# Performance work log

Measured on AMD Instinct MI355X. Metric: run time of the kernel, lower is better.

## Reference

```python
import jax, jax.numpy as jnp
import numpy as np


def setup_inputs() -> dict:
    key = jax.random.key(0)
    ks = jax.random.split(key, 6)
    B = 65536
    x = jax.random.normal(ks[0], (B, 784), dtype=jnp.float32)
    conv_w = jax.random.normal(ks[1], (3, 3), dtype=jnp.float32)
    fc1_w = jax.random.normal(ks[2], (100, 676), dtype=jnp.float32) * (1.0 / np.sqrt(676))
    fc1_b = jax.random.normal(ks[3], (100,), dtype=jnp.float32) * 0.01
    fc2_w = jax.random.normal(ks[4], (10, 100), dtype=jnp.float32) * (1.0 / np.sqrt(100))
    fc2_b = jax.random.normal(ks[5], (10,), dtype=jnp.float32) * 0.01
    return {"x": x, "conv_w": conv_w, "fc1_w": fc1_w, "fc1_b": fc1_b, "fc2_w": fc2_w, "fc2_b": fc2_b}


def reference(x, conv_w, fc1_w, fc1_b, fc2_w, fc2_b):
    B = x.shape[0]
    img = x.reshape(B, 1, 28, 28)  # NCHW, single channel
    kern = conv_w.reshape(1, 1, 3, 3)  # OIHW
    # 'valid' cross-correlation, matching the slicing-based Convolve()
    conv = jax.lax.conv_general_dilated(
        img, kern, window_strides=(1, 1), padding='VALID',
        dimension_numbers=('NCHW', 'OIHW', 'NCHW'))  # [B,1,26,26]
    h = conv.reshape(B, 26 * 26)
    h = jax.nn.relu(h @ fc1_w.T + fc1_b)
    out = h @ fc2_w.T + fc2_b
    return out
```

## Files before the change

### kernel.cpp

```cpp
#include <hip/hip_runtime.h>


typedef short s16x8 __attribute__((ext_vector_type(8)));
typedef float f32x16 __attribute__((ext_vector_type(16)));

#define BM   32
#define CSTR 712
#define HSTR 132
#define KPAD 688

__device__ __forceinline__ unsigned short f2bf(float f) {
    unsigned int u = __builtin_bit_cast(unsigned int, f);
    u = (u + 0x7fffu + ((u >> 16) & 1u)) >> 16;
    return (unsigned short)u;
}

extern "C" __global__ void __launch_bounds__(256, 3)
digit_model_fused(const float* __restrict__ x,
                  const float* __restrict__ cw9,
                  const float* __restrict__ W1,
                  const float* __restrict__ b1,
                  const float* __restrict__ W2,
                  const float* __restrict__ b2,
                  float* __restrict__ out)
{
    __shared__ __align__(16) unsigned char smem[BM * CSTR * 2];
    unsigned short* cbuf = (unsigned short*)smem;
    float*          hbuf = (float*)smem;

    const int tid  = threadIdx.x;
    const int lane = tid & 63;
    const int wv   = tid >> 6;
    const int half = lane >> 5;
    const int ln   = lane & 31;
    const int m0   = blockIdx.x * BM;

    float cw[9];
    #pragma unroll
    for (int i = 0; i < 9; ++i) cw[i] = cw9[i];

    for (int p = tid; p < BM * 18; p += 256) {
        int mi = p / 18, q = p - mi * 18;
        *(unsigned int*)(cbuf + mi * CSTR + 676 + q * 2) = 0u;
    }

    for (int task = tid; task < BM * 26; task += 256) {
        int mi = task / 26, r = task - mi * 26;
        const float* ip = x + (size_t)(m0 + mi) * 784 + r * 28;
        float acc[26];
        #pragma unroll
        for (int c = 0; c < 26; ++c) acc[c] = 0.f;
        #pragma unroll
        for (int dr = 0; dr < 3; ++dr) {
            float rowv[28];
            const float4* rp = (const float4*)(ip + dr * 28);
            #pragma unroll
            for (int q = 0; q < 7; ++q) {
                float4 t = rp[q];
                rowv[q*4+0] = t.x; rowv[q*4+1] = t.y;
                rowv[q*4+2] = t.z; rowv[q*4+3] = t.w;
            }
            #pragma unroll
            for (int dc = 0; dc < 3; ++dc) {
                float w = cw[dr*3+dc];
                #pragma unroll
                for (int c = 0; c < 26; ++c) acc[c] = fmaf(rowv[c+dc], w, acc[c]);
            }
        }
        unsigned short* dst = cbuf + mi * CSTR + r * 26;
        #pragma unroll
        for (int c = 0; c < 26; c += 2) {
            unsigned int u = (unsigned int)f2bf(acc[c])
                           | ((unsigned int)f2bf(acc[c+1]) << 16);
            *(unsigned int*)(dst + c) = u;
        }
    }
    __syncthreads();

    const int n = wv * 32 + ln;
    const bool nvalid = (n < 100);
    f32x16 acc;
    #pragma unroll
    for (int i = 0; i < 16; ++i) acc[i] = 0.f;

    const unsigned short* arow = cbuf + ln * CSTR + half * 8;
    const float* wrow = W1 + (size_t)(nvalid ? n : 0) * 676;

    for (int kc = 0; kc < 43; ++kc) {
        const int k0 = kc * 16 + half * 8;
        uint4 araw = *(const uint4*)(arow + kc * 16);
        s16x8 a = __builtin_bit_cast(s16x8, araw);

        s16x8 b;
        if (nvalid && (k0 + 8 <= 676)) {
            float4 p = *(const float4*)(wrow + k0);
            float4 q = *(const float4*)(wrow + k0 + 4);
            b[0] = (short)f2bf(p.x); b[1] = (short)f2bf(p.y);
            b[2] = (short)f2bf(p.z); b[3] = (short)f2bf(p.w);
            b[4] = (short)f2bf(q.x); b[5] = (short)f2bf(q.y);
            b[6] = (short)f2bf(q.z); b[7] = (short)f2bf(q.w);
        } else {
            #pragma unroll
            for (int j = 0; j < 8; ++j) {
                float v = (nvalid && (k0 + j) < 676) ? wrow[k0 + j] : 0.f;
                b[j] = (short)f2bf(v);
            }
        }
        acc = __builtin_amdgcn_mfma_f32_32x32x16_bf16(a, b, acc, 0, 0, 0);
    }
    __syncthreads();

    const float bias1 = nvalid ? b1[n] : 0.f;
    #pragma unroll
    for (int r = 0; r < 16; ++r) {
        int row = (r & 3) + 8 * (r >> 2) + 4 * half;
        float v = acc[r] + bias1;
        v = v > 0.f ? v : 0.f;
        hbuf[row * HSTR + n] = v;
    }
    __syncthreads();

    for (int p = tid; p < BM * 10; p += 256) {
        int mi = p / 10, o = p - mi * 10;
        const float4* hv = (const float4*)(hbuf + mi * HSTR);
        const float4* w2 = (const float4*)(W2 + o * 100);
        float s = b2[o];
        #pragma unroll
        for (int q = 0; q < 25; ++q) {
            float4 h4 = hv[q], w4 = w2[q];
            s += h4.x*w4.x + h4.y*w4.y + h4.z*w4.z + h4.w*w4.w;
        }
        out[(size_t)(m0 + mi) * 10 + o] = s;
    }
}

extern "C" void kernel_launch(void* const* d_in, const int* in_sizes, int n_in,
                              void* d_out, int out_size, void* d_ws, size_t ws_size,
                              hipStream_t stream) {
    const float* x  = (const float*)d_in[0];
    const float* cw = (const float*)d_in[1];
    const float* W1 = (const float*)d_in[2];
    const float* b1 = (const float*)d_in[3];
    const float* W2 = (const float*)d_in[4];
    const float* b2 = (const float*)d_in[5];
    float* out = (float*)d_out;

    const int B = in_sizes[0] / 784;
    dim3 grid(B / BM), block(256);
    hipLaunchKernelGGL(digit_model_fused, grid, block, 0, stream,
                       x, cw, W1, b1, W2, b2, out);
}
```

Before: 357.5 us.

## Pre-pack W1 to bf16 MFMA layout and split K across two wave groups

Adds a small prep kernel that converts W1 to bf16 in the exact per-lane MFMA B-fragment order, folding the fc1 bias in as an extra K column. The main block gets an LDS column of ones to match, so bias is applied by the MMA. The main kernel grows to 512 threads, with two wave groups each covering half of K; partial sums are reduced through shared memory. The K loop now prefetches the next A/B fragments. The goal is to remove per-block fp32 loading and conversion of W1 and add more latency hiding, at the cost of an extra launch, a reduction step and more barriers.

```diff
diff --git a/kernel.cpp b/kernel.cpp
--- a/kernel.cpp
+++ b/kernel.cpp
@@ -1,13 +1,14 @@
 #include <hip/hip_runtime.h>
 
 
-typedef short s16x8 __attribute__((ext_vector_type(8)));
-typedef float f32x16 __attribute__((ext_vector_type(16)));
+typedef short  s16x8  __attribute__((ext_vector_type(8)));
+typedef float  f32x16 __attribute__((ext_vector_type(16)));
 
 #define BM   32
 #define CSTR 712
 #define HSTR 132
-#define KPAD 688
+#define NT   4
+#define KC   43
 
 __device__ __forceinline__ unsigned short f2bf(float f) {
     unsigned int u = __builtin_bit_cast(unsigned int, f);
@@ -15,60 +16,86 @@
     return (unsigned short)u;
 }
 
-extern "C" __global__ void __launch_bounds__(256, 3)
+extern "C" __global__ void __launch_bounds__(256)
+prep_w1(const float* __restrict__ W1, const float* __restrict__ b1,
+        unsigned short* __restrict__ bw)
+{
+    int id = blockIdx.x * 256 + threadIdx.x;
+    if (id >= NT * KC * 64) return;
+    int lane = id & 63;
+    int kc   = (id >> 6) % KC;
+    int t    = id / (KC * 64);
+    int n    = t * 32 + (lane & 31);
+    int k0   = kc * 16 + (lane >> 5) * 8;
+    unsigned short v[8];
+#pragma unroll
+    for (int j = 0; j < 8; ++j) {
+        int k = k0 + j;
+        float f = 0.f;
+        if (n < 100) {
+            if (k < 676)       f = W1[(size_t)n * 676 + k];
+            else if (k == 676) f = b1[n];
+        }
+        v[j] = f2bf(f);
+    }
+    *(uint4*)(bw + (size_t)id * 8) = *(const uint4*)v;
+}
+
+extern "C" __global__ void __launch_bounds__(512, 6)
 digit_model_fused(const float* __restrict__ x,
                   const float* __restrict__ cw9,
-                  const float* __restrict__ W1,
-                  const float* __restrict__ b1,
+                  const unsigned short* __restrict__ bw,
                   const float* __restrict__ W2,
                   const float* __restrict__ b2,
                   float* __restrict__ out)
 {
     __shared__ __align__(16) unsigned char smem[BM * CSTR * 2];
     unsigned short* cbuf = (unsigned short*)smem;
-    float*          hbuf = (float*)smem;
+    float* pbuf = (float*)smem;
+    float* hbuf = (float*)(smem + 16384);
 
     const int tid  = threadIdx.x;
     const int lane = tid & 63;
     const int wv   = tid >> 6;
+    const int t    = wv & 3;
     const int half = lane >> 5;
     const int ln   = lane & 31;
     const int m0   = blockIdx.x * BM;
 
     float cw[9];
-    #pragma unroll
+#pragma unroll
     for (int i = 0; i < 9; ++i) cw[i] = cw9[i];
 
-    for (int p = tid; p < BM * 18; p += 256) {
+    for (int p = tid; p < BM * 18; p += 512) {
         int mi = p / 18, q = p - mi * 18;
-        *(unsigned int*)(cbuf + mi * CSTR + 676 + q * 2) = 0u;
+        *(unsigned int*)(cbuf + mi * CSTR + 676 + q * 2) = (q == 0) ? 0x3F80u : 0u;
     }
 
-    for (int task = tid; task < BM * 26; task += 256) {
+    for (int task = tid; task < BM * 26; task += 512) {
         int mi = task / 26, r = task - mi * 26;
         const float* ip = x + (size_t)(m0 + mi) * 784 + r * 28;
         float acc[26];
-        #pragma unroll
+#pragma unroll
         for (int c = 0; c < 26; ++c) acc[c] = 0.f;
-        #pragma unroll
+#pragma unroll
         for (int dr = 0; dr < 3; ++dr) {
             float rowv[28];
             const float4* rp = (const float4*)(ip + dr * 28);
-            #pragma unroll
+#pragma unroll
             for (int q = 0; q < 7; ++q) {
-                float4 t = rp[q];
-                rowv[q*4+0] = t.x; rowv[q*4+1] = t.y;
-                rowv[q*4+2] = t.z; rowv[q*4+3] = t.w;
+                float4 v = rp[q];
+                rowv[q*4+0] = v.x; rowv[q*4+1] = v.y;
+                rowv[q*4+2] = v.z; rowv[q*4+3] = v.w;
             }
-            #pragma unroll
+#pragma unroll
             for (int dc = 0; dc < 3; ++dc) {
                 float w = cw[dr*3+dc];
-                #pragma unroll
+#pragma unroll
                 for (int c = 0; c < 26; ++c) acc[c] = fmaf(rowv[c+dc], w, acc[c]);
             }
         }
         unsigned short* dst = cbuf + mi * CSTR + r * 26;
-        #pragma unroll
+#pragma unroll
         for (int c = 0; c < 26; c += 2) {
             unsigned int u = (unsigned int)f2bf(acc[c])
                            | ((unsigned int)f2bf(acc[c+1]) << 16);
@@ -77,55 +104,54 @@
     }
     __syncthreads();
 
-    const int n = wv * 32 + ln;
-    const bool nvalid = (n < 100);
+    const int kbeg = (wv < 4) ? 0 : 21;
+    const int kend = (wv < 4) ? 21 : KC;
+
     f32x16 acc;
-    #pragma unroll
+#pragma unroll
     for (int i = 0; i < 16; ++i) acc[i] = 0.f;
 
     const unsigned short* arow = cbuf + ln * CSTR + half * 8;
-    const float* wrow = W1 + (size_t)(nvalid ? n : 0) * 676;
+    const uint4* bwv = (const uint4*)bw;
 
-    for (int kc = 0; kc < 43; ++kc) {
-        const int k0 = kc * 16 + half * 8;
-        uint4 araw = *(const uint4*)(arow + kc * 16);
-        s16x8 a = __builtin_bit_cast(s16x8, araw);
-
-        s16x8 b;
-        if (nvalid && (k0 + 8 <= 676)) {
-            float4 p = *(const float4*)(wrow + k0);
-            float4 q = *(const float4*)(wrow + k0 + 4);
-            b[0] = (short)f2bf(p.x); b[1] = (short)f2bf(p.y);
-            b[2] = (short)f2bf(p.z); b[3] = (short)f2bf(p.w);
-            b[4] = (short)f2bf(q.x); b[5] = (short)f2bf(q.y);
-            b[6] = (short)f2bf(q.z); b[7] = (short)f2bf(q.w);
-        } else {
-            #pragma unroll
-            for (int j = 0; j < 8; ++j) {
-                float v = (nvalid && (k0 + j) < 676) ? wrow[k0 + j] : 0.f;
-                b[j] = (short)f2bf(v);
-            }
-        }
-        acc = __builtin_amdgcn_mfma_f32_32x32x16_bf16(a, b, acc, 0, 0, 0);
+    uint4 araw = *(const uint4*)(arow + kbeg * 16);
+    uint4 braw = bwv[(t * KC + kbeg) * 64 + lane];
+    for (int kc = kbeg; kc < kend; ++kc) {
+        int kn = (kc + 1 < kend) ? kc + 1 : kc;
+        uint4 na = *(const uint4*)(arow + kn * 16);
+        uint4 nb = bwv[(t * KC + kn) * 64 + lane];
+        acc = __builtin_amdgcn_mfma_f32_32x32x16_bf16(
+                  __builtin_bit_cast(s16x8, araw),
+                  __builtin_bit_cast(s16x8, braw), acc, 0, 0, 0);
+        araw = na; braw = nb;
     }
     __syncthreads();
 
-    const float bias1 = nvalid ? b1[n] : 0.f;
-    #pragma unroll
-    for (int r = 0; r < 16; ++r) {
-        int row = (r & 3) + 8 * (r >> 2) + 4 * half;
-        float v = acc[r] + bias1;
-        v = v > 0.f ? v : 0.f;
-        hbuf[row * HSTR + n] = v;
+    if (wv >= 4) {
+#pragma unroll
+        for (int r = 0; r < 16; ++r) {
+            int row = (r & 3) + 8 * (r >> 2) + 4 * half;
+            pbuf[t * 1024 + row * 32 + ln] = acc[r];
+        }
+    }
+    __syncthreads();
+    if (wv < 4) {
+#pragma unroll
+        for (int r = 0; r < 16; ++r) {
+            int row = (r & 3) + 8 * (r >> 2) + 4 * half;
+            float v = acc[r] + pbuf[t * 1024 + row * 32 + ln];
+            v = v > 0.f ? v : 0.f;
+            hbuf[row * HSTR + t * 32 + ln] = v;
+        }
     }
     __syncthreads();
 
-    for (int p = tid; p < BM * 10; p += 256) {
+    for (int p = tid; p < BM * 10; p += 512) {
         int mi = p / 10, o = p - mi * 10;
         const float4* hv = (const float4*)(hbuf + mi * HSTR);
-        const float4* w2 = (const float4*)(W2 + o * 100);
+        const float4* w2 = (const float4*)(W2 + (size_t)o * 100);
         float s = b2[o];
-        #pragma unroll
+#pragma unroll
         for (int q = 0; q < 25; ++q) {
             float4 h4 = hv[q], w4 = w2[q];
             s += h4.x*w4.x + h4.y*w4.y + h4.z*w4.z + h4.w*w4.w;
@@ -144,9 +170,12 @@
     const float* W2 = (const float*)d_in[4];
     const float* b2 = (const float*)d_in[5];
     float* out = (float*)d_out;
+    unsigned short* bw = (unsigned short*)d_ws;
 
     const int B = in_sizes[0] / 784;
-    dim3 grid(B / BM), block(256);
-    hipLaunchKernelGGL(digit_model_fused, grid, block, 0, stream,
-                       x, cw, W1, b1, W2, b2, out);
+
+    hipLaunchKernelGGL(prep_w1, dim3((NT * KC * 64 + 255) / 256), dim3(256),
+                       0, stream, W1, b1, bw);
+    hipLaunchKernelGGL(digit_model_fused, dim3(B / BM), dim3(512), 0, stream,
+                       x, cw, bw, W2, b2, out);
 }
```

Measured after the change: 348.2 us. 2.6% less time.
